# Performance work log

Measured on AMD Instinct MI355X. Metric: run time of the kernel, lower is better.

Reference implementation:

```python
import jax, jax.numpy as jnp
import numpy as np

N, E, F, H, C = 100000, 1600000, 128, 16, 8


def _gcn_conv(x, src, dst, ew, W, b, n):
    """PyG GCNConv with edge_weight: x@W, add self-loops (weight 1),
    symmetric degree normalization, scatter-add to destination, + bias."""
    h = x @ W                                   # [n, out]
    loop = jnp.arange(n)
    s = jnp.concatenate([src, loop])
    d = jnp.concatenate([dst, loop])
    w = jnp.concatenate([ew, jnp.ones((n,), ew.dtype)])
    deg = jax.ops.segment_sum(w, d, num_segments=n)          # in-degree by edge weight
    dis = jnp.where(deg > 0, jax.lax.rsqrt(deg), 0.0)        # deg^-1/2, inf -> 0
    norm = dis[s] * w * dis[d]                               # [E+n]
    out = jax.ops.segment_sum(h[s] * norm[:, None], d, num_segments=n)
    return out + b


def setup_inputs() -> dict:
    key = jax.random.key(0)
    ks = jax.random.split(key, 7)
    x = jax.random.normal(ks[0], (N, F), dtype=jnp.float32)
    edge_index = jax.random.randint(ks[1], (2, E), 0, N, dtype=jnp.int64)
    edge_attr = jax.random.uniform(ks[2], (E,), dtype=jnp.float32)
    W1 = jax.random.normal(ks[3], (F, H), dtype=jnp.float32) * (1.0 / np.sqrt(F))
    b1 = jnp.zeros((H,), jnp.float32)
    W2 = jax.random.normal(ks[4], (H, C), dtype=jnp.float32) * (1.0 / np.sqrt(H))
    b2 = jnpps = jnp.zeros((C,), jnp.float32)
    return {"x": x, "edge_index": edge_index, "edge_attr": edge_attr,
            "W1": W1, "b1": b1, "W2": W2, "b2": b2}


def reference(x, edge_index, edge_attr, W1, b1, W2, b2):
    n = x.shape[0]
    src, dst = edge_index[0], edge_index[1]
    h = jax.nn.relu(_gcn_conv(x, src, dst, edge_attr, W1, b1, n))
    # F.dropout(training=self.training): identity in eval mode (deterministic ref)
    return _gcn_conv(h, src, dst, edge_attr, W2, b2, n)
```

## Files before the change

### kernel.cpp

```cpp
#include <hip/hip_runtime.h>

#define F_IN  128
#define H_MID 16
#define C_OUT 8
#define XS_PAD (F_IN + 4)
#define TROWS 32
#define CHUNK 4096
#define NBMAX 512
#define CAP   8192
#define GEMM_SHF (2 * TROWS * XS_PAD + F_IN * H_MID)

__global__ void __launch_bounds__(512) k_zero512(int* __restrict__ p) {
    p[threadIdx.x] = 0;
}

__device__ __forceinline__ void gemm1_part(
        const float* __restrict__ x, const float* __restrict__ W1,
        float* __restrict__ h1, int N, int t0, int t1, int j, int S,
        float* __restrict__ arena) {
    float* xs  = arena;
    float* W1s = arena + 2 * TROWS * XS_PAD;
    const int t = threadIdx.x;
    for (int i = t; i < F_IN * H_MID; i += 256) W1s[i] = W1[i];
    const int c  = t & 15;
    const int r0 = t >> 4;
    int tile = t0 + j;
    if (tile >= t1) return;

    float4 st[4];
    auto stage_load = [&](int tl) {
        const float4* xg = reinterpret_cast<const float4*>(x + (long long)tl * TROWS * F_IN);
        const int nfl = ((N - tl * TROWS < TROWS) ? (N - tl * TROWS) : TROWS) * (F_IN / 4);
#pragma unroll
        for (int k = 0; k < 4; ++k) {
            const int i = t + k * 256;
            st[k] = (i < nfl) ? xg[i] : make_float4(0.f, 0.f, 0.f, 0.f);
        }
    };
    auto stage_write = [&](int buf) {
#pragma unroll
        for (int k = 0; k < 4; ++k) {
            const int i = t + k * 256;
            *reinterpret_cast<float4*>(&xs[buf * TROWS * XS_PAD + (i >> 5) * XS_PAD + (i & 31) * 4]) = st[k];
        }
    };

    stage_load(tile);
    stage_write(0);
    __syncthreads();
    int buf = 0;
    while (true) {
        const int next = tile + S;
        if (next < t1) stage_load(next);
        const float* xr0 = &xs[buf * TROWS * XS_PAD + r0 * XS_PAD];
        const float* xr1 = xr0 + 16 * XS_PAD;
        float acc0 = 0.0f, acc1 = 0.0f;
#pragma unroll 4
        for (int k4 = 0; k4 < F_IN / 4; ++k4) {
            const float4 v0 = *reinterpret_cast<const float4*>(&xr0[k4 * 4]);
            const float4 v1 = *reinterpret_cast<const float4*>(&xr1[k4 * 4]);
            const float w0 = W1s[(k4 * 4 + 0) * H_MID + c];
            const float w1 = W1s[(k4 * 4 + 1) * H_MID + c];
            const float w2 = W1s[(k4 * 4 + 2) * H_MID + c];
            const float w3 = W1s[(k4 * 4 + 3) * H_MID + c];
            acc0 = fmaf(v0.x, w0, acc0); acc1 = fmaf(v1.x, w0, acc1);
            acc0 = fmaf(v0.y, w1, acc0); acc1 = fmaf(v1.y, w1, acc1);
            acc0 = fmaf(v0.z, w2, acc0); acc1 = fmaf(v1.z, w2, acc1);
            acc0 = fmaf(v0.w, w3, acc0); acc1 = fmaf(v1.w, w3, acc1);
        }
        const long long row0 = (long long)tile * TROWS + r0;
        const long long row1 = row0 + 16;
        if (row0 < N) h1[row0 * H_MID + c] = acc0;
        if (row1 < N) h1[row1 * H_MID + c] = acc1;
        if (next >= t1) break;
        __syncthreads();
        stage_write(buf ^ 1);
        __syncthreads();
        buf ^= 1;
        tile = next;
    }
}

__global__ void __launch_bounds__(256) k_build_g(
        const int* __restrict__ src, const int* __restrict__ dst,
        const float* __restrict__ ew, int* __restrict__ bcursor,
        int2* __restrict__ bed, int E, int NB,
        const float* __restrict__ x, const float* __restrict__ W1,
        float* __restrict__ h1, int N, int t0, int t1, int NCSR, int NG) {
    struct S {
        int hist[NBMAX], scn[NBMAX], cur[NBMAX], base[NBMAX];
        int2 sorted[CHUNK];
        unsigned short bof[CHUNK];
    };
    union Shm { S s; float g[GEMM_SHF]; };
    __shared__ Shm u;
    const int b = blockIdx.x;
    if (b >= NCSR) { gemm1_part(x, W1, h1, N, t0, t1, b - NCSR, NG, u.g); return; }

    const int t = threadIdx.x;
    const int c0 = b * CHUNK;
    const int n = (E - c0 < CHUNK) ? (E - c0) : CHUNK;

    for (int l = t; l < NBMAX; l += 256) u.s.hist[l] = 0;
    __syncthreads();
    for (int i = t; i < n; i += 256)
        atomicAdd(&u.s.hist[((unsigned)dst[c0 + i]) >> 8], 1);
    __syncthreads();
    u.s.scn[t] = u.s.hist[t];
    u.s.scn[t + 256] = u.s.hist[t + 256];
    __syncthreads();
#pragma unroll
    for (int off = 1; off < 512; off <<= 1) {
        const int i1 = t + 256;
        const int v0 = (t >= off) ? u.s.scn[t - off] : 0;
        const int v1 = u.s.scn[i1 - off];
        __syncthreads();
        u.s.scn[t] += v0;
        u.s.scn[i1] += v1;
        __syncthreads();
    }
    u.s.cur[t] = u.s.scn[t] - u.s.hist[t];
    u.s.cur[t + 256] = u.s.scn[t + 256] - u.s.hist[t + 256];
    __syncthreads();
    for (int i = t; i < n; i += 256) {
        const int s  = src[c0 + i];
        const int d  = dst[c0 + i];
        const float wt = ew[c0 + i];
        const int bk = ((unsigned)d) >> 8;
        const int slot = atomicAdd(&u.s.cur[bk], 1);
        u.s.sorted[slot] = make_int2(s | ((d & 255) << 18), __float_as_int(wt));
        u.s.bof[slot] = (unsigned short)bk;
    }
    __syncthreads();
    for (int l = t; l < NB; l += 256)
        u.s.base[l] = u.s.hist[l] ? (l * CAP + atomicAdd(&bcursor[l], u.s.hist[l])) : 0;
    __syncthreads();
    for (int i = t; i < n; i += 256) {
        const int bk = u.s.bof[i];
        const int excl = u.s.scn[bk] - u.s.hist[bk];
        const int pos = u.s.base[bk] + (i - excl);
        if (pos < (bk + 1) * CAP) bed[pos] = u.s.sorted[i];
    }
}

__global__ void __launch_bounds__(256) k_bsort_g(
        const int2* __restrict__ bed, const int* __restrict__ bcursor,
        int2* __restrict__ rowseg, float* __restrict__ dis,
        int2* __restrict__ ed, int N, int NB,
        const float* __restrict__ x, const float* __restrict__ W1,
        float* __restrict__ h1, int t0, int t1, int NCSR, int NG) {
    struct S { int hist[256], scn[256], cur[256]; float degw[256]; };
    union Shm { S s; float g[GEMM_SHF]; };
    __shared__ Shm u;
    const int b = blockIdx.x;
    if (b >= NCSR) { gemm1_part(x, W1, h1, N, t0, t1, b - NCSR, NG, u.g); return; }

    const int t = threadIdx.x;
    const int r0 = b << 8;
    const int L = (N - r0 < 256) ? (N - r0) : 256;
    const int e0 = b * CAP;
    int M = bcursor[b];
    if (M > CAP) M = CAP;

    u.s.hist[t] = 0;
    u.s.degw[t] = 0.0f;
    __syncthreads();
    for (int i = t; i < M; i += 256) {
        const int2 rec = bed[e0 + i];
        const int dl = ((unsigned)rec.x) >> 18;
        atomicAdd(&u.s.hist[dl], 1);
        atomicAdd(&u.s.degw[dl], __int_as_float(rec.y));
    }
    __syncthreads();
    u.s.scn[t] = u.s.hist[t];
    __syncthreads();
#pragma unroll
    for (int off = 1; off < 256; off <<= 1) {
        int v = (t >= off) ? u.s.scn[t - off] : 0;
        __syncthreads();
        u.s.scn[t] += v;
        __syncthreads();
    }
    const int excl = u.s.scn[t] - u.s.hist[t];
    if (t < L) {
        rowseg[r0 + t] = make_int2(e0 + excl, e0 + u.s.scn[t]);
        dis[r0 + t] = rsqrtf(1.0f + u.s.degw[t]);
    }
    u.s.cur[t] = excl;
    __syncthreads();
    for (int i = t; i < M; i += 256) {
        const int2 rec = bed[e0 + i];
        const int dl = ((unsigned)rec.x) >> 18;
        const int slot = atomicAdd(&u.s.cur[dl], 1);
        ed[e0 + slot] = make_int2(rec.x & 0x3FFFF, rec.y);
    }
}


__global__ void __launch_bounds__(256) k_agg16f(
        const int2* __restrict__ rowseg, const int2* __restrict__ ed,
        const float* __restrict__ h, const float* __restrict__ dis,
        const float* __restrict__ b1, const float* __restrict__ W2,
        float* __restrict__ h2s, int N) {
    __shared__ float W2s[H_MID * C_OUT];
    if (threadIdx.x < H_MID * C_OUT) W2s[threadIdx.x] = W2[threadIdx.x];
    __syncthreads();
    const long long tg = (long long)blockIdx.x * 256 + threadIdx.x;
    const int node = (int)(tg >> 4);
    const int c = (int)(tg & 15);
    if (node >= N) return;
    const int2 seg = rowseg[node];
    const float dn = dis[node];
    float a0 = h[(long long)node * H_MID + c] * dn;
    float a1 = 0.f, a2 = 0.f, a3 = 0.f;
    int e = seg.x;
    for (; e + 3 < seg.y; e += 4) {
        const int2 p0 = ed[e],     p1 = ed[e + 1];
        const int2 p2 = ed[e + 2], p3 = ed[e + 3];
        const float w0 = __int_as_float(p0.y) * dis[p0.x];
        const float w1 = __int_as_float(p1.y) * dis[p1.x];
        const float w2 = __int_as_float(p2.y) * dis[p2.x];
        const float w3 = __int_as_float(p3.y) * dis[p3.x];
        a0 = fmaf(h[(long long)p0.x * H_MID + c], w0, a0);
        a1 = fmaf(h[(long long)p1.x * H_MID + c], w1, a1);
        a2 = fmaf(h[(long long)p2.x * H_MID + c], w2, a2);
        a3 = fmaf(h[(long long)p3.x * H_MID + c], w3, a3);
    }
    for (; e < seg.y; ++e) {
        const int2 p = ed[e];
        a0 = fmaf(h[(long long)p.x * H_MID + c], __int_as_float(p.y) * dis[p.x], a0);
    }
    float r = fmaf((a0 + a1) + (a2 + a3), dn, b1[c]);
    r = fmaxf(r, 0.0f);
    float h2 = 0.0f;
#pragma unroll
    for (int cc = 0; cc < H_MID; ++cc) {
        const float rc = __shfl(r, cc, 16);
        h2 = fmaf(rc, W2s[cc * C_OUT + (c & 7)], h2);
    }
    if (c < C_OUT) h2s[(long long)node * C_OUT + c] = h2 * dn;
}

__global__ void __launch_bounds__(256) k_agg8(
        const int2* __restrict__ rowseg, const int2* __restrict__ ed,
        const float* __restrict__ h, const float* __restrict__ dis,
        const float* __restrict__ b2, float* __restrict__ out, int N) {
    const long long tg = (long long)blockIdx.x * 256 + threadIdx.x;
    const int node = (int)(tg >> 3);
    const int c = (int)(tg & 7);
    if (node >= N) return;
    const int2 seg = rowseg[node];
    float a0 = h[(long long)node * C_OUT + c];
    float a1 = 0.f, a2 = 0.f, a3 = 0.f;
    int e = seg.x;
    for (; e + 3 < seg.y; e += 4) {
        const int2 p0 = ed[e],     p1 = ed[e + 1];
        const int2 p2 = ed[e + 2], p3 = ed[e + 3];
        a0 = fmaf(h[(long long)p0.x * C_OUT + c], __int_as_float(p0.y), a0);
        a1 = fmaf(h[(long long)p1.x * C_OUT + c], __int_as_float(p1.y), a1);
        a2 = fmaf(h[(long long)p2.x * C_OUT + c], __int_as_float(p2.y), a2);
        a3 = fmaf(h[(long long)p3.x * C_OUT + c], __int_as_float(p3.y), a3);
    }
    for (; e < seg.y; ++e) {
        const int2 p = ed[e];
        a0 = fmaf(h[(long long)p.x * C_OUT + c], __int_as_float(p.y), a0);
    }
    out[(long long)node * C_OUT + c] = fmaf((a0 + a1) + (a2 + a3), dis[node], b2[c]);
}

__global__ void k_init_deg(float* __restrict__ deg, int N) {
    int i = blockIdx.x * blockDim.x + threadIdx.x;
    if (i < N) deg[i] = 1.0f;
}
__global__ void k_scatter_deg(const int* __restrict__ dst, const float* __restrict__ ew,
                              float* __restrict__ deg, int E) {
    int e = blockIdx.x * blockDim.x + threadIdx.x;
    if (e < E) atomicAdd(&deg[dst[e]], ew[e]);
}
__global__ void k_rsqrt(float* __restrict__ deg, int N) {
    int i = blockIdx.x * blockDim.x + threadIdx.x;
    if (i < N) {
        float v = deg[i];
        deg[i] = (v > 0.0f) ? rsqrtf(v) : 0.0f;
    }
}
__global__ void k_gemm1_r2(const float* __restrict__ x, const float* __restrict__ W1,
                           const float* __restrict__ b1, const float* __restrict__ dis,
                           float* __restrict__ h1, float* __restrict__ a1, int N) {
    __shared__ float W1s[F_IN * H_MID];
    for (int i = threadIdx.x; i < F_IN * H_MID; i += blockDim.x) W1s[i] = W1[i];
    __syncthreads();
    const int c   = threadIdx.x & 15;
    const int lr  = threadIdx.x >> 4;
    const int rpb = blockDim.x >> 4;
    for (long long row = (long long)blockIdx.x * rpb + lr; row < N;
         row += (long long)gridDim.x * rpb) {
        const float4* xr = reinterpret_cast<const float4*>(x + row * F_IN);
        float acc = 0.0f;
#pragma unroll
        for (int k4 = 0; k4 < F_IN / 4; ++k4) {
            float4 v = xr[k4];
            acc = fmaf(v.x, W1s[(k4 * 4 + 0) * H_MID + c], acc);
            acc = fmaf(v.y, W1s[(k4 * 4 + 1) * H_MID + c], acc);
            acc = fmaf(v.z, W1s[(k4 * 4 + 2) * H_MID + c], acc);
            acc = fmaf(v.w, W1s[(k4 * 4 + 3) * H_MID + c], acc);
        }
        h1[row * H_MID + c] = acc;
        float di = dis[row];
        a1[row * H_MID + c] = fmaf(acc, di * di, b1[c]);
    }
}
template <int CH>
__global__ void k_agg_at(const int* __restrict__ src, const int* __restrict__ dst,
                         const float* __restrict__ ew, const float* __restrict__ dis,
                         const float* __restrict__ h, float* __restrict__ out, long long E) {
    const int LOG = (CH == 16) ? 4 : 3;
    const long long total  = E << LOG;
    const long long stride = (long long)gridDim.x * blockDim.x;
    for (long long idx = (long long)blockIdx.x * blockDim.x + threadIdx.x; idx < total;
         idx += stride) {
        const long long e = idx >> LOG;
        const int c = (int)(idx & (CH - 1));
        const int s = src[e];
        const int d = dst[e];
        const float norm = dis[s] * ew[e] * dis[d];
        atomicAdd(out + (long long)d * CH + c, h[(long long)s * CH + c] * norm);
    }
}
__global__ void k_gemm2_r2(const float* __restrict__ a1, const float* __restrict__ W2,
                           const float* __restrict__ b2, const float* __restrict__ dis,
                           float* __restrict__ h2, float* __restrict__ out, int N) {
    __shared__ float W2s[H_MID * C_OUT];
    if (threadIdx.x < H_MID * C_OUT) W2s[threadIdx.x] = W2[threadIdx.x];
    __syncthreads();
    const int c   = threadIdx.x & 7;
    const int lr  = threadIdx.x >> 3;
    const int rpb = blockDim.x >> 3;
    for (long long row = (long long)blockIdx.x * rpb + lr; row < N;
         row += (long long)gridDim.x * rpb) {
        const float4* ar = reinterpret_cast<const float4*>(a1 + row * H_MID);
        float acc = 0.0f;
#pragma unroll
        for (int k4 = 0; k4 < H_MID / 4; ++k4) {
            float4 v = ar[k4];
            acc = fmaf(fmaxf(v.x, 0.0f), W2s[(k4 * 4 + 0) * C_OUT + c], acc);
            acc = fmaf(fmaxf(v.y, 0.0f), W2s[(k4 * 4 + 1) * C_OUT + c], acc);
            acc = fmaf(fmaxf(v.z, 0.0f), W2s[(k4 * 4 + 2) * C_OUT + c], acc);
            acc = fmaf(fmaxf(v.w, 0.0f), W2s[(k4 * 4 + 3) * C_OUT + c], acc);
        }
        h2[row * C_OUT + c] = acc;
        float di = dis[row];
        out[row * C_OUT + c] = fmaf(acc, di * di, b2[c]);
    }
}

extern "C" void kernel_launch(void* const* d_in, const int* in_sizes, int n_in,
                              void* d_out, int out_size, void* d_ws, size_t ws_size,
                              hipStream_t stream) {
    const float* x  = (const float*)d_in[0];
    const int*   ei = (const int*)d_in[1];
    const float* ew = (const float*)d_in[2];
    const float* W1 = (const float*)d_in[3];
    const float* b1 = (const float*)d_in[4];
    const float* W2 = (const float*)d_in[5];
    const float* b2 = (const float*)d_in[6];
    float* out = (float*)d_out;

    const int H   = in_sizes[4];
    const int Fin = in_sizes[3] / H;
    const int N   = in_sizes[0] / Fin;
    const int E   = in_sizes[2];
    const int* src = ei;
    const int* dst = ei + E;
    (void)n_in; (void)out_size;

    char* ws = (char*)d_ws;
    size_t off = 0;
    auto alloc = [&](size_t bytes) {
        void* p = ws + off;
        off = (off + bytes + 255) & ~(size_t)255;
        return p;
    };
    float* dis    = (float*)alloc((size_t)N * sizeof(float));
    float* h1     = (float*)alloc((size_t)N * H_MID * sizeof(float));
    int2*  rowseg = (int2*)alloc((size_t)N * sizeof(int2));
    int*   bcursor= (int*)alloc(NBMAX * sizeof(int));
    const int NB  = (N + 255) >> 8;
    int2*  bed    = (int2*)alloc((size_t)NB * CAP * sizeof(int2));
    int2*  ed     = (int2*)alloc((size_t)NB * CAP * sizeof(int2));
    float* h2s = (float*)bed;
    const size_t needed = off;

    const int B = 256;
    const int NCH = (E + CHUNK - 1) / CHUNK;
    const bool fast_ok = (needed <= ws_size) && (N <= 131072) && (NB <= NBMAX) &&
                         (2 * ((E + NB - 1) / NB) <= CAP) &&
                         ((size_t)NB * CAP * sizeof(int2) >= (size_t)N * C_OUT * sizeof(float));

    if (fast_ok) {
        const int ntiles = (N + TROWS - 1) / TROWS;
        const int GB_S = (NCH < 704) ? (768 - NCH) : 64;
        const int GB_B = (NB  < 704) ? (768 - NB)  : 64;
        const int tA = (int)((long long)ntiles * 60 / 100);

        k_zero512<<<1, 512, 0, stream>>>(bcursor);
        k_build_g<<<NCH + GB_S, B, 0, stream>>>(src, dst, ew, bcursor, bed, E, NB,
                                                x, W1, h1, N, 0, tA, NCH, GB_S);
        k_bsort_g<<<NB + GB_B, B, 0, stream>>>(bed, bcursor, rowseg, dis, ed, N, NB,
                                               x, W1, h1, tA, ntiles, NB, GB_B);
        k_agg16f<<<(int)(((long long)N * H_MID + B - 1) / B), B, 0, stream>>>(
            rowseg, ed, h1, dis, b1, W2, h2s, N);
        k_agg8<<<(int)(((long long)N * C_OUT + B - 1) / B), B, 0, stream>>>(
            rowseg, ed, h2s, dis, b2, out, N);
    } else {
        off = 0;
        float* disF = (float*)alloc((size_t)N * sizeof(float));
        float* h1F  = (float*)alloc((size_t)N * H_MID * sizeof(float));
        float* a1F  = (float*)alloc((size_t)N * H_MID * sizeof(float));
        float* h2   = (float*)alloc((size_t)N * C_OUT * sizeof(float));
        k_init_deg<<<(N + B - 1) / B, B, 0, stream>>>(disF, N);
        k_scatter_deg<<<(E + B - 1) / B, B, 0, stream>>>(dst, ew, disF, E);
        k_rsqrt<<<(N + B - 1) / B, B, 0, stream>>>(disF, N);
        k_gemm1_r2<<<(N + 15) / 16, B, 0, stream>>>(x, W1, b1, disF, h1F, a1F, N);
        k_agg_at<H_MID><<<8192, B, 0, stream>>>(src, dst, ew, disF, h1F, a1F, E);
        k_gemm2_r2<<<(N + 31) / 32, B, 0, stream>>>(a1F, W2, b2, disF, h2, out, N);
        k_agg_at<C_OUT><<<8192, B, 0, stream>>>(src, dst, ew, disF, h2, out, E);
    }
}
```

Baseline: 111.5 us.

## Single-buffer GEMM1 tiles, shrink edge chunk, and enlarge co-scheduled GEMM grids

The GEMM1 helper drops its register-staged double buffer for a simple single-buffered load-sync-compute loop, which halves its shared-memory footprint. The edge bucketing chunk is reduced from 4096 to 3072 edges per block, giving more, smaller build blocks. The GEMM filler blocks in both co-scheduled kernels are raised so each kernel launches about 1024 blocks total, and the tile split between the two kernels is now proportional to their GEMM block counts. The aim is higher occupancy and better balance between the CSR-building work and the overlapped GEMM, at the cost of losing load/compute overlap inside each GEMM block.

```diff
diff --git a/kernel.cpp b/kernel.cpp
--- a/kernel.cpp
+++ b/kernel.cpp
@@ -5,10 +5,10 @@
 #define C_OUT 8
 #define XS_PAD (F_IN + 4)
 #define TROWS 32
-#define CHUNK 4096
+#define CHUNK 3072
 #define NBMAX 512
 #define CAP   8192
-#define GEMM_SHF (2 * TROWS * XS_PAD + F_IN * H_MID)
+#define GEMM_SHF (TROWS * XS_PAD + F_IN * H_MID)
 
 __global__ void __launch_bounds__(512) k_zero512(int* __restrict__ p) {
     p[threadIdx.x] = 0;
@@ -19,40 +19,24 @@
         float* __restrict__ h1, int N, int t0, int t1, int j, int S,
         float* __restrict__ arena) {
     float* xs  = arena;
-    float* W1s = arena + 2 * TROWS * XS_PAD;
+    float* W1s = arena + TROWS * XS_PAD;
     const int t = threadIdx.x;
     for (int i = t; i < F_IN * H_MID; i += 256) W1s[i] = W1[i];
     const int c  = t & 15;
     const int r0 = t >> 4;
-    int tile = t0 + j;
-    if (tile >= t1) return;
-
-    float4 st[4];
-    auto stage_load = [&](int tl) {
-        const float4* xg = reinterpret_cast<const float4*>(x + (long long)tl * TROWS * F_IN);
-        const int nfl = ((N - tl * TROWS < TROWS) ? (N - tl * TROWS) : TROWS) * (F_IN / 4);
+
+    for (int tile = t0 + j; tile < t1; tile += S) {
+        __syncthreads();
+        const float4* xg = reinterpret_cast<const float4*>(x + (long long)tile * TROWS * F_IN);
+        const int nfl = ((N - tile * TROWS < TROWS) ? (N - tile * TROWS) : TROWS) * (F_IN / 4);
 #pragma unroll
         for (int k = 0; k < 4; ++k) {
             const int i = t + k * 256;
-            st[k] = (i < nfl) ? xg[i] : make_float4(0.f, 0.f, 0.f, 0.f);
+            const float4 v = (i < nfl) ? xg[i] : make_float4(0.f, 0.f, 0.f, 0.f);
+            *reinterpret_cast<float4*>(&xs[(i >> 5) * XS_PAD + (i & 31) * 4]) = v;
         }
-    };
-    auto stage_write = [&](int buf) {
-#pragma unroll
-        for (int k = 0; k < 4; ++k) {
-            const int i = t + k * 256;
-            *reinterpret_cast<float4*>(&xs[buf * TROWS * XS_PAD + (i >> 5) * XS_PAD + (i & 31) * 4]) = st[k];
-        }
-    };
-
-    stage_load(tile);
-    stage_write(0);
-    __syncthreads();
-    int buf = 0;
-    while (true) {
-        const int next = tile + S;
-        if (next < t1) stage_load(next);
-        const float* xr0 = &xs[buf * TROWS * XS_PAD + r0 * XS_PAD];
+        __syncthreads();
+        const float* xr0 = &xs[r0 * XS_PAD];
         const float* xr1 = xr0 + 16 * XS_PAD;
         float acc0 = 0.0f, acc1 = 0.0f;
 #pragma unroll 4
@@ -72,12 +56,6 @@
         const long long row1 = row0 + 16;
         if (row0 < N) h1[row0 * H_MID + c] = acc0;
         if (row1 < N) h1[row1 * H_MID + c] = acc1;
-        if (next >= t1) break;
-        __syncthreads();
-        stage_write(buf ^ 1);
-        __syncthreads();
-        buf ^= 1;
-        tile = next;
     }
 }
 
@@ -399,9 +377,9 @@
 
     if (fast_ok) {
         const int ntiles = (N + TROWS - 1) / TROWS;
-        const int GB_S = (NCH < 704) ? (768 - NCH) : 64;
-        const int GB_B = (NB  < 704) ? (768 - NB)  : 64;
-        const int tA = (int)((long long)ntiles * 60 / 100);
+        const int GB_S = (NCH < 960) ? (1024 - NCH) : 64;
+        const int GB_B = (NB  < 960) ? (1024 - NB)  : 64;
+        const int tA = (int)((long long)ntiles * GB_S / (GB_S + GB_B));
 
         k_zero512<<<1, 512, 0, stream>>>(bcursor);
         k_build_g<<<NCH + GB_S, B, 0, stream>>>(src, dst, ew, bcursor, bed, E, NB,
```

New measurement: 114.5 us. 2.7% more time.
